# Kernel tuning notes

Measured on AMD Instinct MI355X. Metric: run time of the kernel, lower is better.

The kernel has to match this reference:

```python
import jax, jax.numpy as jnp
import numpy as np

B, T, C = 4, 2048, 1024
H = 16
HD = C // H  # 64


def setup_inputs() -> dict:
    key = jax.random.key(0)
    ks = jax.random.split(key, 4)
    x = jax.random.normal(ks[0], (B, T, C), dtype=jnp.float32)
    # c_attn: Linear(C, 3C, bias=False)  (qkv_bias=False)
    w_attn = jax.random.normal(ks[1], (C, 3 * C), dtype=jnp.float32) / np.sqrt(C)
    # c_proj: Linear(C, C) with bias (nn.Linear default)
    w_proj = jax.random.normal(ks[2], (C, C), dtype=jnp.float32) / np.sqrt(C)
    b_proj = jax.random.normal(ks[3], (C,), dtype=jnp.float32) * 0.01
    return {"x": x, "w_attn": w_attn, "w_proj": w_proj, "b_proj": b_proj}


def reference(x, w_attn, w_proj, b_proj):
    b, t, c = x.shape
    qkv = x @ w_attn  # [B,T,3C]
    q, k, v = jnp.split(qkv, 3, axis=-1)
    # [B,H,T,HD]
    q = q.reshape(b, t, H, HD).transpose(0, 2, 1, 3)
    k = k.reshape(b, t, H, HD).transpose(0, 2, 1, 3)
    v = v.reshape(b, t, H, HD).transpose(0, 2, 1, 3)
    scale = 1.0 / np.sqrt(HD)
    attn = jnp.einsum('bhqd,bhkd->bhqk', q, k) * scale  # [B,H,T,T]
    causal = jnp.tril(jnp.ones((t, t), dtype=bool))
    attn = jnp.where(causal, attn, -jnp.inf)
    attn = jax.nn.softmax(attn, axis=-1)
    out = jnp.einsum('bhqk,bhkd->bhqd', attn, v)  # [B,H,T,HD]
    out = out.transpose(0, 2, 1, 3).reshape(b, t, c)
    return out @ w_proj + b_proj
```

## Files before the change

### kernel.cpp

```cpp
#include <hip/hip_runtime.h>

#define BB 4
#define TT 2048
#define CC 1024
#define C3 3072
#define HH 16
#define HD 64
#define BT 8192

typedef __bf16 bf16x8 __attribute__((ext_vector_type(8)));
typedef float floatx4 __attribute__((ext_vector_type(4)));
typedef unsigned short u16;

__device__ __forceinline__ u16 f2bf(float f) {
  union { float f; unsigned u; } a; a.f = f;
  return (u16)((a.u + 0x7fffu + ((a.u >> 16) & 1u)) >> 16);
}
__device__ __forceinline__ bf16x8 ld8(const u16* p) { return *(const bf16x8*)p; }
__device__ __forceinline__ floatx4 mfma16(bf16x8 a, bf16x8 b, floatx4 c) {
  return __builtin_amdgcn_mfma_f32_16x16x32_bf16(a, b, c, 0, 0, 0);
}

__global__ __launch_bounds__(256) void tobf16_kernel(const float4* __restrict__ src,
                                                     ushort4* __restrict__ dst, int n4) {
  int i = blockIdx.x * 256 + threadIdx.x;
  if (i >= n4) return;
  float4 v = src[i];
  ushort4 o; o.x = f2bf(v.x); o.y = f2bf(v.y); o.z = f2bf(v.z); o.w = f2bf(v.w);
  dst[i] = o;
}

__global__ __launch_bounds__(256) void transpose_bf16_kernel(const float* __restrict__ src,
                                                             u16* __restrict__ dst,
                                                             int K, int N) {
  __shared__ float s[64][65];
  const int t = threadIdx.x;
  const int r = t >> 4;
  const int c = (t & 15) * 4;
  const int k0 = blockIdx.y * 64, n0 = blockIdx.x * 64;
#pragma unroll
  for (int i = 0; i < 4; ++i) {
    float4 v = *(const float4*)&src[(size_t)(k0 + r + i * 16) * N + n0 + c];
    s[r + i * 16][c + 0] = v.x; s[r + i * 16][c + 1] = v.y;
    s[r + i * 16][c + 2] = v.z; s[r + i * 16][c + 3] = v.w;
  }
  __syncthreads();
#pragma unroll
  for (int i = 0; i < 4; ++i) {
    const int nn = r + i * 16;
    ushort4 o;
    o.x = f2bf(s[c + 0][nn]); o.y = f2bf(s[c + 1][nn]);
    o.z = f2bf(s[c + 2][nn]); o.w = f2bf(s[c + 3][nn]);
    *(ushort4*)&dst[(size_t)(n0 + nn) * K + k0 + c] = o;
  }
}

template<int MODE>
__global__ __launch_bounds__(256) void gemm_kernel(
    const u16* __restrict__ A, const u16* __restrict__ B,
    const float* __restrict__ bias, float* __restrict__ outf,
    u16* __restrict__ qk, u16* __restrict__ vT,
    int M, int N, int K) {
  __shared__ u16 smem[2][2][4096];

  const int t = threadIdx.x;
  const int w = t >> 6, lane = t & 63, lr = lane & 15, qd = lane >> 4;
  const int wm = w >> 1, wn = w & 1;
  const int m0 = blockIdx.y * 128, n0 = blockIdx.x * 128;

  const int sr = t >> 2;
  const int sc = (t & 3) * 8;
  const int so = sr * 32 + sc;
  const u16* Ag = A + (size_t)(m0 + sr) * K + sc;
  const u16* Bg = B + (size_t)(n0 + sr) * K + sc;

  floatx4 acc[4][4] = {};

  uint4 rA0, rA1, rB0, rB1;
  rA0 = *(const uint4*)(Ag);
  rA1 = *(const uint4*)(Ag + (size_t)64 * K);
  rB0 = *(const uint4*)(Bg);
  rB1 = *(const uint4*)(Bg + (size_t)64 * K);

  for (int k0 = 0; k0 < K; k0 += 32) {
    const int p = (k0 >> 5) & 1;
    u16* sA = &smem[p][0][0];
    u16* sB = &smem[p][1][0];
    *(uint4*)&sA[so]        = rA0;
    *(uint4*)&sA[2048 + so] = rA1;
    *(uint4*)&sB[so]        = rB0;
    *(uint4*)&sB[2048 + so] = rB1;
    __syncthreads();
    if (k0 + 32 < K) {
      rA0 = *(const uint4*)(Ag + k0 + 32);
      rA1 = *(const uint4*)(Ag + (size_t)64 * K + k0 + 32);
      rB0 = *(const uint4*)(Bg + k0 + 32);
      rB1 = *(const uint4*)(Bg + (size_t)64 * K + k0 + 32);
    }

    bf16x8 af[4], bf[4];
#pragma unroll
    for (int mj = 0; mj < 4; ++mj) af[mj] = ld8(&sA[(wm * 64 + mj * 16 + lr) * 32 + qd * 8]);
#pragma unroll
    for (int nj = 0; nj < 4; ++nj) bf[nj] = ld8(&sB[(wn * 64 + nj * 16 + lr) * 32 + qd * 8]);
#pragma unroll
    for (int mj = 0; mj < 4; ++mj)
#pragma unroll
      for (int nj = 0; nj < 4; ++nj)
        acc[mj][nj] = mfma16(af[mj], bf[nj], acc[mj][nj]);
  }

  const int rowg0 = m0 + wm * 64;
  const int colg0 = n0 + wn * 64;
  if constexpr (MODE == 2) {
#pragma unroll
    for (int nj = 0; nj < 4; ++nj) {
      const int col = colg0 + nj * 16 + lr;
      const float bv = bias[col];
#pragma unroll
      for (int mj = 0; mj < 4; ++mj)
#pragma unroll
        for (int i = 0; i < 4; ++i)
          outf[(size_t)(rowg0 + mj * 16 + qd * 4 + i) * N + col] = acc[mj][nj][i] + bv;
    }
  } else {
    __syncthreads();
    u16* Tw = &smem[0][0][0] + w * (32 * 72);
    const bool isV = (n0 >= 2 * CC);
    if (!isV) {
#pragma unroll
      for (int half = 0; half < 2; ++half) {
#pragma unroll
        for (int m2 = 0; m2 < 2; ++m2)
#pragma unroll
          for (int nj = 0; nj < 4; ++nj)
#pragma unroll
            for (int i = 0; i < 4; ++i)
              Tw[(m2 * 16 + qd * 4 + i) * 72 + nj * 16 + lr] =
                  f2bf(acc[half * 2 + m2][nj][i]);
#pragma unroll
        for (int s = 0; s < 4; ++s) {
          const int rl = s * 8 + (lane >> 3);
          const int c0 = (lane & 7) * 8;
          *(bf16x8*)&qk[(size_t)(rowg0 + half * 32 + rl) * (2 * CC) + colg0 + c0] =
              ld8(&Tw[rl * 72 + c0]);
        }
      }
    } else {
      const int bI = m0 >> 11;
      const int tbase = (m0 & (TT - 1)) + wm * 64;
      const int dim0 = colg0 - 2 * CC;
#pragma unroll
      for (int half = 0; half < 2; ++half) {
#pragma unroll
        for (int n2 = 0; n2 < 2; ++n2)
#pragma unroll
          for (int mj = 0; mj < 4; ++mj)
#pragma unroll
            for (int i = 0; i < 4; ++i)
              Tw[(n2 * 16 + lr) * 72 + mj * 16 + qd * 4 + i] =
                  f2bf(acc[mj][half * 2 + n2][i]);
#pragma unroll
        for (int s = 0; s < 4; ++s) {
          const int dl = s * 8 + (lane >> 3);
          const int t0 = (lane & 7) * 8;
          *(bf16x8*)&vT[((size_t)(bI << 10) + dim0 + half * 32 + dl) * TT + tbase + t0] =
              ld8(&Tw[dl * 72 + t0]);
        }
      }
    }
  }
}

__global__ __launch_bounds__(256, 3) void attn_kernel(const u16* __restrict__ qk,
                                                      const u16* __restrict__ vT,
                                                      u16* __restrict__ att) {
  __shared__ u16 sKV[2][4][64 * 32];
  __shared__ u16 sP[4 * 16 * 72];

  const int t = threadIdx.x;
  const int w = t >> 6, lane = t & 63, lr = lane & 15, qd = lane >> 4;
  const int qtile = 31 - blockIdx.y;
  const int bh = blockIdx.x;
  const int b = bh >> 4, h = bh & 15;
  const int q0 = qtile * 64;
  const u16* qbase = qk + (size_t)b * TT * (2 * CC);

  const u16* qp = qbase + (size_t)(q0 + w * 16 + lr) * (2 * CC) + h * HD;
  const bf16x8 qf0 = ld8(qp + qd * 8);
  const bf16x8 qf1 = ld8(qp + 32 + qd * 8);

  const int sr = t >> 2, sc = (t & 3) * 8;
  const int so = sr * 32 + sc;
  const u16* Kg = qbase + (size_t)sr * (2 * CC) + CC + h * HD + sc;
  const u16* Vg = vT + ((size_t)bh * HD + sr) * TT + sc;

  float lsum = 0.f;
  floatx4 o[4] = {};
  const float SC = 0.125f * 1.44269504089f;
  u16* Pw = &sP[w * 16 * 72];
  const int myq = q0 + w * 16 + lr;

  uint4 rK0, rK1, rV0, rV1;
  rK0 = *(const uint4*)(Kg);
  rK1 = *(const uint4*)(Kg + 32);
  rV0 = *(const uint4*)(Vg);
  rV1 = *(const uint4*)(Vg + 32);

  for (int kt = 0; kt <= qtile; ++kt) {
    u16* base = &sKV[kt & 1][0][0];
    *(uint4*)&base[so]        = rK0;
    *(uint4*)&base[2048 + so] = rK1;
    *(uint4*)&base[4096 + so] = rV0;
    *(uint4*)&base[6144 + so] = rV1;
    __syncthreads();
    if (kt < qtile) {
      const int kn = (kt + 1) * 64;
      rK0 = *(const uint4*)(Kg + (size_t)kn * (2 * CC));
      rK1 = *(const uint4*)(Kg + (size_t)kn * (2 * CC) + 32);
      rV0 = *(const uint4*)(Vg + kn);
      rV1 = *(const uint4*)(Vg + kn + 32);
    }

    const u16* sK0 = &sKV[kt & 1][0][0];
    const u16* sK1 = &sKV[kt & 1][1][0];
    const u16* sV0 = &sKV[kt & 1][2][0];
    const u16* sV1 = &sKV[kt & 1][3][0];

    floatx4 s[4] = {};
#pragma unroll
    for (int j = 0; j < 4; ++j) {
      bf16x8 kf0 = ld8(&sK0[(j * 16 + lr) * 32 + qd * 8]);
      bf16x8 kf1 = ld8(&sK1[(j * 16 + lr) * 32 + qd * 8]);
      s[j] = mfma16(kf0, qf0, s[j]);
      s[j] = mfma16(kf1, qf1, s[j]);
    }

    const bool diag = (kt == qtile);
#pragma unroll
    for (int j = 0; j < 4; ++j) {
      float p[4];
#pragma unroll
      for (int i = 0; i < 4; ++i) {
        p[i] = exp2f(s[j][i] * SC);
        if (diag) {
          const int key = kt * 64 + j * 16 + qd * 4 + i;
          p[i] = (key <= myq) ? p[i] : 0.f;
        }
        lsum += p[i];
      }
      uint2 pk;
      pk.x = __builtin_amdgcn_perm(__float_as_uint(p[1]), __float_as_uint(p[0]), 0x07060302);
      pk.y = __builtin_amdgcn_perm(__float_as_uint(p[3]), __float_as_uint(p[2]), 0x07060302);
      *(uint2*)&Pw[lr * 72 + j * 16 + qd * 4] = pk;
    }

    const bf16x8 pf0 = ld8(&Pw[lr * 72 + qd * 8]);
    const bf16x8 pf1 = ld8(&Pw[lr * 72 + 32 + qd * 8]);

#pragma unroll
    for (int j = 0; j < 4; ++j) {
      bf16x8 vf0 = ld8(&sV0[(j * 16 + lr) * 32 + qd * 8]);
      bf16x8 vf1 = ld8(&sV1[(j * 16 + lr) * 32 + qd * 8]);
      o[j] = mfma16(pf0, vf0, o[j]);
      o[j] = mfma16(pf1, vf1, o[j]);
    }
  }

  lsum += __shfl_xor(lsum, 16);
  lsum += __shfl_xor(lsum, 32);
  float linv[4];
#pragma unroll
  for (int i = 0; i < 4; ++i) linv[i] = 1.0f / __shfl(lsum, qd * 4 + i);

#pragma unroll
  for (int j = 0; j < 4; ++j)
#pragma unroll
    for (int i = 0; i < 4; ++i) {
      const size_t row = (size_t)b * TT + q0 + w * 16 + qd * 4 + i;
      att[row * CC + h * HD + j * 16 + lr] = f2bf(o[j][i] * linv[i]);
    }
}

extern "C" void kernel_launch(void* const* d_in, const int* in_sizes, int n_in,
                              void* d_out, int out_size, void* d_ws, size_t ws_size,
                              hipStream_t stream) {
  const float* x      = (const float*)d_in[0];
  const float* w_attn = (const float*)d_in[1];
  const float* w_proj = (const float*)d_in[2];
  const float* b_proj = (const float*)d_in[3];
  float* out = (float*)d_out;

  char* ws = (char*)d_ws;
  u16* xb  = (u16*)(ws + 0);
  u16* waT = (u16*)(ws + 16777216);
  u16* wpT = (u16*)(ws + 23068672);
  u16* qk  = (u16*)(ws + 25165824);
  u16* vT  = (u16*)(ws + 58720256);
  u16* att = (u16*)(ws + 75497472);

  tobf16_kernel<<<8192, 256, 0, stream>>>((const float4*)x, (ushort4*)xb, 2097152);
  transpose_bf16_kernel<<<dim3(48, 16), 256, 0, stream>>>(w_attn, waT, CC, C3);
  transpose_bf16_kernel<<<dim3(16, 16), 256, 0, stream>>>(w_proj, wpT, CC, CC);

  gemm_kernel<1><<<dim3(24, 64), 256, 0, stream>>>(xb, waT, nullptr, nullptr, qk, vT,
                                                   BT, C3, CC);
  attn_kernel<<<dim3(64, 32), 256, 0, stream>>>(qk, vT, att);

  gemm_kernel<2><<<dim3(8, 64), 256, 0, stream>>>(att, wpT, b_proj, out, nullptr, nullptr,
                                                  BT, CC, CC);
}
```

Baseline: 259.4 us.

## Process two 64-row query tiles per attention block to reuse K/V tiles

Each attention block now handles 128 query rows as two 64-row fragments sharing every K/V tile loaded into shared memory. The grid is halved and K/V fragments are read from LDS once per iteration into registers, then used for both query fragments. Fully masked fragments are skipped and the mask is applied only near the diagonal. This roughly halves global K/V traffic, but raises register pressure (two sets of accumulators plus K/V fragment registers), which may cut occupancy, and gives fewer blocks with more causal imbalance.

```diff
diff --git a/kernel.cpp b/kernel.cpp
--- a/kernel.cpp
+++ b/kernel.cpp
@@ -180,26 +180,29 @@
 
   const int t = threadIdx.x;
   const int w = t >> 6, lane = t & 63, lr = lane & 15, qd = lane >> 4;
-  const int qtile = 31 - blockIdx.y;
+  const int qtile = 15 - blockIdx.y;
   const int bh = blockIdx.x;
   const int b = bh >> 4, h = bh & 15;
-  const int q0 = qtile * 64;
+  const int q0 = qtile * 128;
   const u16* qbase = qk + (size_t)b * TT * (2 * CC);
 
-  const u16* qp = qbase + (size_t)(q0 + w * 16 + lr) * (2 * CC) + h * HD;
-  const bf16x8 qf0 = ld8(qp + qd * 8);
-  const bf16x8 qf1 = ld8(qp + 32 + qd * 8);
+  bf16x8 qf[2][2];
+#pragma unroll
+  for (int f = 0; f < 2; ++f) {
+    const u16* qp = qbase + (size_t)(q0 + f * 64 + w * 16 + lr) * (2 * CC) + h * HD;
+    qf[f][0] = ld8(qp + qd * 8);
+    qf[f][1] = ld8(qp + 32 + qd * 8);
+  }
 
   const int sr = t >> 2, sc = (t & 3) * 8;
   const int so = sr * 32 + sc;
   const u16* Kg = qbase + (size_t)sr * (2 * CC) + CC + h * HD + sc;
   const u16* Vg = vT + ((size_t)bh * HD + sr) * TT + sc;
 
-  float lsum = 0.f;
-  floatx4 o[4] = {};
+  float lsum[2] = {0.f, 0.f};
+  floatx4 o[2][4] = {};
   const float SC = 0.125f * 1.44269504089f;
   u16* Pw = &sP[w * 16 * 72];
-  const int myq = q0 + w * 16 + lr;
 
   uint4 rK0, rK1, rV0, rV1;
   rK0 = *(const uint4*)(Kg);
@@ -207,14 +210,15 @@
   rV0 = *(const uint4*)(Vg);
   rV1 = *(const uint4*)(Vg + 32);
 
-  for (int kt = 0; kt <= qtile; ++kt) {
+  const int ktmax = 2 * qtile + 1;
+  for (int kt = 0; kt <= ktmax; ++kt) {
     u16* base = &sKV[kt & 1][0][0];
     *(uint4*)&base[so]        = rK0;
     *(uint4*)&base[2048 + so] = rK1;
     *(uint4*)&base[4096 + so] = rV0;
     *(uint4*)&base[6144 + so] = rV1;
     __syncthreads();
-    if (kt < qtile) {
+    if (kt < ktmax) {
       const int kn = (kt + 1) * 64;
       rK0 = *(const uint4*)(Kg + (size_t)kn * (2 * CC));
       rK1 = *(const uint4*)(Kg + (size_t)kn * (2 * CC) + 32);
@@ -227,59 +231,71 @@
     const u16* sV0 = &sKV[kt & 1][2][0];
     const u16* sV1 = &sKV[kt & 1][3][0];
 
-    floatx4 s[4] = {};
+    bf16x8 kf[4][2], vf[4][2];
 #pragma unroll
     for (int j = 0; j < 4; ++j) {
-      bf16x8 kf0 = ld8(&sK0[(j * 16 + lr) * 32 + qd * 8]);
-      bf16x8 kf1 = ld8(&sK1[(j * 16 + lr) * 32 + qd * 8]);
-      s[j] = mfma16(kf0, qf0, s[j]);
-      s[j] = mfma16(kf1, qf1, s[j]);
-    }
-
-    const bool diag = (kt == qtile);
-#pragma unroll
-    for (int j = 0; j < 4; ++j) {
-      float p[4];
+      kf[j][0] = ld8(&sK0[(j * 16 + lr) * 32 + qd * 8]);
+      kf[j][1] = ld8(&sK1[(j * 16 + lr) * 32 + qd * 8]);
+      vf[j][0] = ld8(&sV0[(j * 16 + lr) * 32 + qd * 8]);
+      vf[j][1] = ld8(&sV1[(j * 16 + lr) * 32 + qd * 8]);
+    }
+
+    const int kt64 = kt * 64;
+#pragma unroll
+    for (int f = 0; f < 2; ++f) {
+      const int qb = q0 + f * 64 + w * 16;
+      if (kt64 > qb + 15) continue;
+      floatx4 s[4] = {};
+#pragma unroll
+      for (int j = 0; j < 4; ++j) {
+        s[j] = mfma16(kf[j][0], qf[f][0], s[j]);
+        s[j] = mfma16(kf[j][1], qf[f][1], s[j]);
+      }
+      const bool needmask = (kt64 + 63 > qb);
+      const int myq = qb + lr;
+#pragma unroll
+      for (int j = 0; j < 4; ++j) {
+        float p[4];
+#pragma unroll
+        for (int i = 0; i < 4; ++i) {
+          p[i] = exp2f(s[j][i] * SC);
+          if (needmask) {
+            const int key = kt64 + j * 16 + qd * 4 + i;
+            p[i] = (key <= myq) ? p[i] : 0.f;
+          }
+          lsum[f] += p[i];
+        }
+        uint2 pk;
+        pk.x = __builtin_amdgcn_perm(__float_as_uint(p[1]), __float_as_uint(p[0]), 0x07060302);
+        pk.y = __builtin_amdgcn_perm(__float_as_uint(p[3]), __float_as_uint(p[2]), 0x07060302);
+        *(uint2*)&Pw[lr * 72 + j * 16 + qd * 4] = pk;
+      }
+      const bf16x8 pf0 = ld8(&Pw[lr * 72 + qd * 8]);
+      const bf16x8 pf1 = ld8(&Pw[lr * 72 + 32 + qd * 8]);
+#pragma unroll
+      for (int j = 0; j < 4; ++j) {
+        o[f][j] = mfma16(pf0, vf[j][0], o[f][j]);
+        o[f][j] = mfma16(pf1, vf[j][1], o[f][j]);
+      }
+    }
+  }
+
+#pragma unroll
+  for (int f = 0; f < 2; ++f) {
+    float ls = lsum[f];
+    ls += __shfl_xor(ls, 16);
+    ls += __shfl_xor(ls, 32);
+    float linv[4];
+#pragma unroll
+    for (int i = 0; i < 4; ++i) linv[i] = 1.0f / __shfl(ls, qd * 4 + i);
+#pragma unroll
+    for (int j = 0; j < 4; ++j)
 #pragma unroll
       for (int i = 0; i < 4; ++i) {
-        p[i] = exp2f(s[j][i] * SC);
-        if (diag) {
-          const int key = kt * 64 + j * 16 + qd * 4 + i;
-          p[i] = (key <= myq) ? p[i] : 0.f;
-        }
-        lsum += p[i];
-      }
-      uint2 pk;
-      pk.x = __builtin_amdgcn_perm(__float_as_uint(p[1]), __float_as_uint(p[0]), 0x07060302);
-      pk.y = __builtin_amdgcn_perm(__float_as_uint(p[3]), __float_as_uint(p[2]), 0x07060302);
-      *(uint2*)&Pw[lr * 72 + j * 16 + qd * 4] = pk;
-    }
-
-    const bf16x8 pf0 = ld8(&Pw[lr * 72 + qd * 8]);
-    const bf16x8 pf1 = ld8(&Pw[lr * 72 + 32 + qd * 8]);
-
-#pragma unroll
-    for (int j = 0; j < 4; ++j) {
-      bf16x8 vf0 = ld8(&sV0[(j * 16 + lr) * 32 + qd * 8]);
-      bf16x8 vf1 = ld8(&sV1[(j * 16 + lr) * 32 + qd * 8]);
-      o[j] = mfma16(pf0, vf0, o[j]);
-      o[j] = mfma16(pf1, vf1, o[j]);
-    }
-  }
-
-  lsum += __shfl_xor(lsum, 16);
-  lsum += __shfl_xor(lsum, 32);
-  float linv[4];
-#pragma unroll
-  for (int i = 0; i < 4; ++i) linv[i] = 1.0f / __shfl(lsum, qd * 4 + i);
-
-#pragma unroll
-  for (int j = 0; j < 4; ++j)
-#pragma unroll
-    for (int i = 0; i < 4; ++i) {
-      const size_t row = (size_t)b * TT + q0 + w * 16 + qd * 4 + i;
-      att[row * CC + h * HD + j * 16 + lr] = f2bf(o[j][i] * linv[i]);
-    }
+        const size_t row = (size_t)b * TT + q0 + f * 64 + w * 16 + qd * 4 + i;
+        att[row * CC + h * HD + j * 16 + lr] = f2bf(o[f][j][i] * linv[i]);
+      }
+  }
 }
 
 extern "C" void kernel_launch(void* const* d_in, const int* in_sizes, int n_in,
@@ -305,7 +321,7 @@
 
   gemm_kernel<1><<<dim3(24, 64), 256, 0, stream>>>(xb, waT, nullptr, nullptr, qk, vT,
                                                    BT, C3, CC);
-  attn_kernel<<<dim3(64, 32), 256, 0, stream>>>(qk, vT, att);
+  attn_kernel<<<dim3(64, 16), 256, 0, stream>>>(qk, vT, att);
 
   gemm_kernel<2><<<dim3(8, 64), 256, 0, stream>>>(att, wpT, b_proj, out, nullptr, nullptr,
                                                   BT, CC, CC);
```

Result: slower. 278.6 us (+7.4%).
